# Kernel tuning notes

Measured on AMD Instinct MI355X. Metric: run time of the kernel, lower is better.

## Reference

```python
import jax, jax.numpy as jnp
import numpy as np

MARGIN = 0.0
B, N = 4096, 128


def setup_inputs() -> dict:
    key = jax.random.key(0)
    k1, k2 = jax.random.split(key)
    scores = jax.random.normal(k1, (B * N,), dtype=jnp.float32)
    # werRank: per-utterance ranking of hypothesis indices by WER (a permutation of 0..N-1)
    werRank = jnp.argsort(jax.random.uniform(k2, (B, N)), axis=1).astype(jnp.int32)
    return {"scores": scores, "nBestIndex": N, "werRank": werRank}


def reference(scores, nBestIndex, werRank):
    n = nBestIndex  # uniform segment length (python int)
    s2 = scores.reshape(-1, n)                       # [B, N] per-utterance scores
    s = jnp.take_along_axis(s2, werRank, axis=1)     # scores ordered by WER rank
    # MarginRankingLoss with target=1: relu(margin - (pos - neg)) = relu(neg - pos + margin)
    # pos = s[:, j], neg = s[:, k] for k > j
    pair = jnp.maximum(s[:, None, :] - s[:, :, None] + MARGIN, 0.0)  # [B, j, k]
    mask = jnp.triu(jnp.ones((n, n), dtype=s.dtype), k=1)            # k > j
    per_j = (pair * mask).sum(-1)                    # [B, N] sum over neg set
    counts = (n - 1 - jnp.arange(n - 1)).astype(s.dtype)  # |neg set| for j < N-1
    # reduction='mean' per (utterance, j) pair-group, then accumulated (summed)
    total = (per_j[:, : n - 1] / counts).sum()
    return total.reshape(1)
```

## Files before the change

kernel.cpp:

```cpp
#include <hip/hip_runtime.h>

#define N_HYP 128
#define BLOCK 256
#define WAVES 4

__global__ __launch_bounds__(BLOCK) void margin_loss_k1(
    const float* __restrict__ scores, const int* __restrict__ werRank,
    float* __restrict__ partials, int B) {
  __shared__ float s_lds[WAVES][N_HYP];

  const int tid  = threadIdx.x;
  const int lane = tid & 63;
  const int wid  = tid >> 6;
  const int u = blockIdx.x * WAVES + wid;
  const bool valid = (u < B);
  const size_t base = (size_t)(valid ? u : 0) * N_HYP;

  const int r0 = werRank[base + lane];
  const int r1 = werRank[base + lane + 64];
  const float sj0 = scores[base + r0];
  const float sj1 = scores[base + r1];
  s_lds[wid][lane]      = sj0;
  s_lds[wid][lane + 64] = sj1;

  const float4* srow = (const float4*)&s_lds[wid][0];
  float a0 = 0.f, b0 = 0.f, a1 = 0.f, b1 = 0.f;

#pragma unroll
  for (int q = 0; q < 16; ++q) {
    const float4 sv = srow[q];
    const int k = q * 4;
    a0 += (k + 0 > lane) ? fmaxf(sv.x - sj0, 0.f) : 0.f;
    b0 += (k + 1 > lane) ? fmaxf(sv.y - sj0, 0.f) : 0.f;
    a0 += (k + 2 > lane) ? fmaxf(sv.z - sj0, 0.f) : 0.f;
    b0 += (k + 3 > lane) ? fmaxf(sv.w - sj0, 0.f) : 0.f;
  }
#pragma unroll
  for (int q = 16; q < 32; ++q) {
    const float4 sv = srow[q];
    const int km = q * 4 - 64;
    a0 += fmaxf(sv.x - sj0, 0.f);
    b0 += fmaxf(sv.y - sj0, 0.f);
    a0 += fmaxf(sv.z - sj0, 0.f);
    b0 += fmaxf(sv.w - sj0, 0.f);
    a1 += (km + 0 > lane) ? fmaxf(sv.x - sj1, 0.f) : 0.f;
    b1 += (km + 1 > lane) ? fmaxf(sv.y - sj1, 0.f) : 0.f;
    a1 += (km + 2 > lane) ? fmaxf(sv.z - sj1, 0.f) : 0.f;
    b1 += (km + 3 > lane) ? fmaxf(sv.w - sj1, 0.f) : 0.f;
  }

  const float acc0 = a0 + b0;
  const float acc1 = a1 + b1;
  const float w0 = 1.0f / (float)(N_HYP - 1 - lane);
  const float w1 = (lane < 63) ? 1.0f / (float)(63 - lane)
                               : 0.0f;
  float val = acc0 * w0 + acc1 * w1;

  for (int off = 32; off > 0; off >>= 1) val += __shfl_down(val, off, 64);
  if (lane == 0 && valid) partials[u] = val;
}

__global__ __launch_bounds__(256) void margin_loss_k2(
    const float* __restrict__ p, int n, float* __restrict__ out) {
  float v = 0.f;
  const int n4 = n >> 2;
  const float4* p4 = (const float4*)p;
  for (int i = threadIdx.x; i < n4; i += 256) {
    const float4 t = p4[i];
    v += (t.x + t.y) + (t.z + t.w);
  }
  for (int i = (n & ~3) + threadIdx.x; i < n; i += 256) v += p[i];
  for (int off = 32; off > 0; off >>= 1) v += __shfl_down(v, off, 64);
  __shared__ float ws[4];
  if ((threadIdx.x & 63) == 0) ws[threadIdx.x >> 6] = v;
  __syncthreads();
  if (threadIdx.x == 0) out[0] = (ws[0] + ws[1]) + (ws[2] + ws[3]);
}

extern "C" void kernel_launch(void* const* d_in, const int* in_sizes, int n_in,
                              void* d_out, int out_size, void* d_ws, size_t ws_size,
                              hipStream_t stream) {
  const float* scores  = (const float*)d_in[0];
  const int*   werRank = (const int*)d_in[2];
  float* out = (float*)d_out;
  float* partials = (float*)d_ws;
  const int B = in_sizes[0] / N_HYP;

  const int nblocks = (B + WAVES - 1) / WAVES;
  margin_loss_k1<<<nblocks, BLOCK, 0, stream>>>(scores, werRank, partials, B);
  margin_loss_k2<<<1, 256, 0, stream>>>(partials, B, out);
}
```

Baseline: 14.53 us.

## Fuse final reduction into main kernel via last-block atomic counter

Merges the two-kernel scheme into one kernel. Each block reduces its four waves to one partial and bumps a global atomic counter, and the last block to finish sums all partials and writes the output. This removes the second kernel launch and the gap between launches, but adds a hipMemsetAsync to reset the counter plus a threadfence and atomic in every block.

```diff
diff --git a/kernel.cpp b/kernel.cpp
--- a/kernel.cpp
+++ b/kernel.cpp
@@ -4,10 +4,13 @@
 #define BLOCK 256
 #define WAVES 4
 
-__global__ __launch_bounds__(BLOCK) void margin_loss_k1(
+__global__ __launch_bounds__(BLOCK) void margin_loss_fused(
     const float* __restrict__ scores, const int* __restrict__ werRank,
-    float* __restrict__ partials, int B) {
+    float* __restrict__ partials, unsigned int* __restrict__ counter,
+    float* __restrict__ out, int B, int nblocks) {
   __shared__ float s_lds[WAVES][N_HYP];
+  __shared__ float wave_sum[WAVES];
+  __shared__ bool amLast;
 
   const int tid  = threadIdx.x;
   const int lane = tid & 63;
@@ -49,32 +52,41 @@
     b1 += (km + 3 > lane) ? fmaxf(sv.w - sj1, 0.f) : 0.f;
   }
 
-  const float acc0 = a0 + b0;
-  const float acc1 = a1 + b1;
   const float w0 = 1.0f / (float)(N_HYP - 1 - lane);
   const float w1 = (lane < 63) ? 1.0f / (float)(63 - lane)
                                : 0.0f;
-  float val = acc0 * w0 + acc1 * w1;
+  float val = (a0 + b0) * w0 + (a1 + b1) * w1;
+  if (!valid) val = 0.f;
 
   for (int off = 32; off > 0; off >>= 1) val += __shfl_down(val, off, 64);
-  if (lane == 0 && valid) partials[u] = val;
-}
+  if (lane == 0) wave_sum[wid] = val;
+  __syncthreads();
 
-__global__ __launch_bounds__(256) void margin_loss_k2(
-    const float* __restrict__ p, int n, float* __restrict__ out) {
-  float v = 0.f;
-  const int n4 = n >> 2;
-  const float4* p4 = (const float4*)p;
-  for (int i = threadIdx.x; i < n4; i += 256) {
-    const float4 t = p4[i];
-    v += (t.x + t.y) + (t.z + t.w);
+  if (tid == 0) {
+    const float bs = (wave_sum[0] + wave_sum[1]) + (wave_sum[2] + wave_sum[3]);
+    partials[blockIdx.x] = bs;
+    __threadfence();
+    const unsigned prev = atomicAdd(counter, 1u);
+    amLast = (prev == (unsigned)(nblocks - 1));
   }
-  for (int i = (n & ~3) + threadIdx.x; i < n; i += 256) v += p[i];
-  for (int off = 32; off > 0; off >>= 1) v += __shfl_down(v, off, 64);
-  __shared__ float ws[4];
-  if ((threadIdx.x & 63) == 0) ws[threadIdx.x >> 6] = v;
   __syncthreads();
-  if (threadIdx.x == 0) out[0] = (ws[0] + ws[1]) + (ws[2] + ws[3]);
+
+  if (amLast) {
+    __threadfence();
+    float v = 0.f;
+    const int n4 = nblocks >> 2;
+    const float4* p4 = (const float4*)partials;
+    for (int i = tid; i < n4; i += BLOCK) {
+      const float4 t = p4[i];
+      v += (t.x + t.y) + (t.z + t.w);
+    }
+    for (int i = (nblocks & ~3) + tid; i < nblocks; i += BLOCK) v += partials[i];
+    for (int off = 32; off > 0; off >>= 1) v += __shfl_down(v, off, 64);
+    __syncthreads();
+    if ((tid & 63) == 0) wave_sum[tid >> 6] = v;
+    __syncthreads();
+    if (tid == 0) out[0] = (wave_sum[0] + wave_sum[1]) + (wave_sum[2] + wave_sum[3]);
+  }
 }
 
 extern "C" void kernel_launch(void* const* d_in, const int* in_sizes, int n_in,
@@ -83,10 +95,13 @@
   const float* scores  = (const float*)d_in[0];
   const int*   werRank = (const int*)d_in[2];
   float* out = (float*)d_out;
+  const int B = in_sizes[0] / N_HYP;
+  const int nblocks = (B + WAVES - 1) / WAVES;
+
   float* partials = (float*)d_ws;
-  const int B = in_sizes[0] / N_HYP;
+  unsigned int* counter = (unsigned int*)((char*)d_ws + ((nblocks * 4 + 255) & ~255));
 
-  const int nblocks = (B + WAVES - 1) / WAVES;
-  margin_loss_k1<<<nblocks, BLOCK, 0, stream>>>(scores, werRank, partials, B);
-  margin_loss_k2<<<1, 256, 0, stream>>>(partials, B, out);
+  hipMemsetAsync(counter, 0, sizeof(unsigned int), stream);
+  margin_loss_fused<<<nblocks, BLOCK, 0, stream>>>(scores, werRank, partials,
+                                                   counter, out, B, nblocks);
 }
```

New measurement: 36.28 us. 150% more time.
